# Kernel tuning notes

Measured on AMD Instinct MI355X. Metric: run time of the kernel, lower is better.

Reference implementation:

```python
import jax, jax.numpy as jnp
import numpy as np
import math

B, C, H, W = 8, 512, 32, 32
ENC = 1024
L2 = 64
NH = 8
GROUPS = 32
EPS = 1e-5

def group_norm(x, gamma, beta):
    # x: (B, C, L) GroupNorm with 32 groups (float32)
    b, c, l = x.shape
    xg = x.reshape(b, GROUPS, (c // GROUPS) * l)
    mean = xg.mean(-1, keepdims=True)
    var = xg.var(-1, keepdims=True)
    xn = ((xg - mean) * jax.lax.rsqrt(var + EPS)).reshape(b, c, l)
    return xn * gamma[None, :, None] + beta[None, :, None]

def conv1x1(w, bias, x):
    # conv_nd(1, in, out, 1): w (out, in), x (B, in, L) -> (B, out, L)
    return jnp.einsum('oc,bcl->bol', w, x) + bias[None, :, None]

def setup_inputs() -> dict:
    key = jax.random.key(0)
    ks = jax.random.split(key, 16)
    s = lambda fan_in: 1.0 / math.sqrt(fan_in)
    inp = {
        'x': jax.random.normal(ks[0], (B, C, H, W), jnp.float32),
        'xf_out': jax.random.normal(ks[1], (B, ENC, L2), jnp.float32),
        'obj_class_embedding': jax.random.normal(ks[2], (B, ENC, L2), jnp.float32),
        'obj_bbox_embedding': jax.random.normal(ks[3], (B, ENC, L2), jnp.float32),
        'image_patch_bbox_embedding': jax.random.normal(ks[4], (B, ENC, H * W), jnp.float32),
        'key_padding_mask': jax.random.bernoulli(ks[5], 0.3, (B, L2)),
        'qkv_w': jax.random.normal(ks[6], (3 * C, C), jnp.float32) * s(C),
        'qkv_b': jnp.zeros((3 * C,), jnp.float32),
        'g_qkv': jnp.ones((C,), jnp.float32),
        'b_qkv': jnp.zeros((C,), jnp.float32),
        'lc_w': jax.random.normal(ks[7], (2 * C, ENC), jnp.float32) * s(ENC),
        'lc_b': jnp.zeros((2 * C,), jnp.float32),
        'lp_w': jax.random.normal(ks[8], (C, ENC), jnp.float32) * s(ENC),
        'lp_b': jnp.zeros((C,), jnp.float32),
        'g_obj': jnp.ones((ENC,), jnp.float32),
        'b_obj': jnp.zeros((ENC,), jnp.float32),
        'g_lpos': jnp.ones((C,), jnp.float32),
        'b_lpos': jnp.zeros((C,), jnp.float32),
        'g_ipos': jnp.ones((C,), jnp.float32),
        'b_ipos': jnp.zeros((C,), jnp.float32),
        # proj_out is zero-initialized in the original (zero_module); use random
        # weights so the projection math is exercised non-trivially.
        'proj_w': jax.random.normal(ks[9], (C, C), jnp.float32) * s(C),
        'proj_b': jnp.zeros((C,), jnp.float32),
    }
    return inp

def reference(x, xf_out, obj_class_embedding, obj_bbox_embedding,
              image_patch_bbox_embedding, key_padding_mask,
              qkv_w, qkv_b, g_qkv, b_qkv, lc_w, lc_b, lp_w, lp_b,
              g_obj, b_obj, g_lpos, b_lpos, g_ipos, b_ipos, proj_w, proj_b):
    b, c, h, w = x.shape
    L1 = h * w
    d = C // NH
    xf = x.reshape(b, c, L1)

    qkv = conv1x1(qkv_w, qkv_b, group_norm(xf, g_qkv, b_qkv))  # (B, 3C, L1)
    q, k, v = jnp.split(qkv, 3, axis=1)
    q = q.reshape(b * NH, d, L1)
    k = k.reshape(b * NH, d, L1)
    v = v.reshape(b * NH, d, L1)

    ipp = group_norm(conv1x1(lp_w, lp_b, image_patch_bbox_embedding), g_ipos, b_ipos)
    ipp = ipp.reshape(b * NH, d, L1)

    q_img = jnp.concatenate([q, ipp], axis=1)  # (B*H, 2d, L1)
    k_img = jnp.concatenate([k, ipp], axis=1)

    lpe = group_norm(conv1x1(lp_w, lp_b, obj_bbox_embedding), g_lpos, b_lpos)
    lpe = lpe.reshape(b * NH, d, L2)

    lce = (xf_out + group_norm(obj_class_embedding, g_obj, b_obj)) / 2
    kl, vl = jnp.split(conv1x1(lc_w, lc_b, lce), 2, axis=1)
    kl = kl.reshape(b * NH, d, L2)
    vl = vl.reshape(b * NH, d, L2)
    k_layout = jnp.concatenate([kl, lpe], axis=1)  # (B*H, 2d, L2)

    k_mix = jnp.concatenate([k_img, k_layout], axis=2)  # (B*H, 2d, L1+L2)
    v_mix = jnp.concatenate([v, vl], axis=2)             # (B*H, d, L1+L2)

    mask = jnp.concatenate([jnp.zeros((b, L1), bool), key_padding_mask], axis=1)  # (B, L1+L2)

    scale = 1.0 / math.sqrt(math.sqrt(2 * C // NH))
    attn = jnp.einsum('bct,bcs->bts', q_img * scale, k_mix * scale)  # (B*H, L1, L1+L2)
    attn = attn.reshape(b, NH, L1, L1 + L2)
    attn = jnp.where(mask[:, None, None, :], -jnp.inf, attn)
    attn = jax.nn.softmax(attn.astype(jnp.float32), axis=-1).astype(attn.dtype)
    attn = attn.reshape(b * NH, L1, L1 + L2)

    out = jnp.einsum('bts,bcs->bct', attn, v_mix).reshape(b, C, L1)
    hproj = conv1x1(proj_w, proj_b, out)
    return (xf + hproj).reshape(b, c, h, w)
```

## Files before the change

### kernel.cpp

```cpp
#include <hip/hip_runtime.h>
#include <math.h>

#define NB 8
#define NC 512
#define NL1 1024
#define NL2 64
#define NLKV 1088
#define NENC 1024
#define EPSV 1e-5f
#define SCALE2 0.08838834764831845f
#define SCALE2Q 0.12752425f
#define DEFER_THR 11.5415603f

typedef _Float16 half8 __attribute__((ext_vector_type(8)));
typedef _Float16 half4 __attribute__((ext_vector_type(4)));
typedef __fp16 fp16x2 __attribute__((ext_vector_type(2)));
typedef float f32x4 __attribute__((ext_vector_type(4)));
typedef float f32x16 __attribute__((ext_vector_type(16)));

__device__ __forceinline__ void gload16(const _Float16* g, _Float16* l) {
  __builtin_amdgcn_global_load_lds(
      (const __attribute__((address_space(1))) void*)g,
      (__attribute__((address_space(3))) void*)l, 16, 0, 0);
}

__device__ __forceinline__ unsigned int pkrtz(float a, float b) {
  union { fp16x2 hh; unsigned int uu; } cv;
  cv.hh = __builtin_amdgcn_cvt_pkrtz(a, b);
  return cv.uu;
}

__device__ __forceinline__ float fast_exp2(float x) {
  return __builtin_amdgcn_exp2f(x);
}

__global__ __launch_bounds__(256) void k_init(
    const float* __restrict__ x, const float* __restrict__ obj,
    float* __restrict__ xm, float* __restrict__ xr,
    float* __restrict__ om, float* __restrict__ orr,
    const float* __restrict__ qkv_w, _Float16* __restrict__ w16qkv,
    const float* __restrict__ lp_w, _Float16* __restrict__ w16lp,
    const float* __restrict__ proj_w, _Float16* __restrict__ w16proj,
    const float* __restrict__ lc_w, _Float16* __restrict__ w16lc)
{
  int bid = blockIdx.x;
  if (bid < 512) {
    const float* p; float* meanp; float* rstdp; int n, bg;
    if (bid < 256) {
      bg = bid;
      int b = bg >> 5, g = bg & 31;
      p = x + ((size_t)b * 512 + (size_t)g * 16) * 1024;
      n = 16 * 1024; meanp = xm; rstdp = xr;
    } else {
      bg = bid - 256;
      int b = bg >> 5, g = bg & 31;
      p = obj + ((size_t)b * 1024 + (size_t)g * 32) * 64;
      n = 32 * 64; meanp = om; rstdp = orr;
    }
    float s = 0.f, s2 = 0.f;
    for (int i = threadIdx.x; i < n; i += 256) { float v = p[i]; s += v; s2 += v * v; }
    #pragma unroll
    for (int o = 32; o > 0; o >>= 1) { s += __shfl_down(s, o); s2 += __shfl_down(s2, o); }
    __shared__ float rs[4], rq[4];
    int lane = threadIdx.x & 63, w = threadIdx.x >> 6;
    if (lane == 0) { rs[w] = s; rq[w] = s2; }
    __syncthreads();
    if (threadIdx.x == 0) {
      float S = rs[0] + rs[1] + rs[2] + rs[3];
      float Q = rq[0] + rq[1] + rq[2] + rq[3];
      float m = S / n;
      float v = Q / n - m * m;
      if (v < 0.f) v = 0.f;
      meanp[bg] = m;
      rstdp[bg] = rsqrtf(v + EPSV);
    }
  } else {
    int cb = bid - 512;
    const float* s; _Float16* d; int i4;
    if (cb < 768)        { s = qkv_w;  d = w16qkv;  i4 = cb * 256 + threadIdx.x; }
    else if (cb < 1280)  { s = lp_w;   d = w16lp;   i4 = (cb - 768) * 256 + threadIdx.x; }
    else if (cb < 1536)  { s = proj_w; d = w16proj; i4 = (cb - 1280) * 256 + threadIdx.x; }
    else                 { s = lc_w;   d = w16lc;   i4 = (cb - 1536) * 256 + threadIdx.x; }
    float4 v = *(const float4*)&s[(size_t)i4 * 4];
    half4 o; o.x = (_Float16)v.x; o.y = (_Float16)v.y; o.z = (_Float16)v.z; o.w = (_Float16)v.w;
    *(half4*)&d[(size_t)i4 * 4] = o;
  }
}

__global__ __launch_bounds__(256) void k_prep(
    const float* __restrict__ x, const float* __restrict__ xm, const float* __restrict__ xr,
    const float* __restrict__ g_qkv, const float* __restrict__ b_qkv, _Float16* __restrict__ xT,
    const float* __restrict__ ipbe, _Float16* __restrict__ ipbeT,
    const float* __restrict__ xf_out, const float* __restrict__ obj_class,
    const float* __restrict__ obj_bbox,
    const float* __restrict__ om, const float* __restrict__ orr,
    const float* __restrict__ g_obj, const float* __restrict__ b_obj,
    _Float16* __restrict__ lceT, _Float16* __restrict__ objT)
{
  __shared__ _Float16 tile[64][72];
  const int bid = blockIdx.x;
  const int tl = threadIdx.x & 63;
  if (bid < 1024) {
    const int tt = bid & 15, ct = (bid >> 4) & 7, b = bid >> 7;
    const int c0 = ct * 64, t0 = tt * 64;
    const int cp = threadIdx.x >> 6;
    #pragma unroll
    for (int i = 0; i < 16; i++) {
      int c = c0 + i * 4 + cp;
      float v = x[((size_t)b * NC + c) * NL1 + t0 + tl];
      int g = c >> 4;
      float ga = g_qkv[c] * xr[b * 32 + g];
      float be = b_qkv[c] - xm[b * 32 + g] * ga;
      tile[tl][i * 4 + cp] = (_Float16)(v * ga + be);
    }
    __syncthreads();
    int tr = threadIdx.x >> 2, c16 = (threadIdx.x & 3) * 16;
    _Float16* dst = xT + ((size_t)b * 1024 + t0 + tr) * 512 + c0 + c16;
    *(half8*)dst = *(half8*)&tile[tr][c16];
    *(half8*)(dst + 8) = *(half8*)&tile[tr][c16 + 8];
  } else if (bid < 3072) {
    const int e2 = bid - 1024;
    const int tt = e2 & 15, et = (e2 >> 4) & 15, b = e2 >> 8;
    const int e0 = et * 64, t0 = tt * 64;
    const int ep = threadIdx.x >> 6;
    #pragma unroll
    for (int i = 0; i < 16; i++) {
      int e = e0 + i * 4 + ep;
      tile[tl][i * 4 + ep] = (_Float16)ipbe[((size_t)b * 1024 + e) * 1024 + t0 + tl];
    }
    __syncthreads();
    int tr = threadIdx.x >> 2, c16 = (threadIdx.x & 3) * 16;
    _Float16* d = ipbeT + ((size_t)b * 1024 + t0 + tr) * 1024 + e0 + c16;
    *(half8*)d = *(half8*)&tile[tr][c16];
    *(half8*)(d + 8) = *(half8*)&tile[tr][c16 + 8];
  } else {
    const int e2 = bid - 3072;
    const int et = e2 & 15, which = (e2 >> 4) & 1, b = e2 >> 5;
    const int e0 = et * 64;
    const int ep = threadIdx.x >> 6;
    if (which == 0) {
      #pragma unroll
      for (int i = 0; i < 16; i++) {
        int e = e0 + i * 4 + ep;
        size_t idx = ((size_t)b * 1024 + e) * 64 + tl;
        int g = e >> 5;
        float xn = (obj_class[idx] - om[b * 32 + g]) * orr[b * 32 + g] * g_obj[e] + b_obj[e];
        tile[tl][i * 4 + ep] = (_Float16)(0.5f * (xf_out[idx] + xn));
      }
    } else {
      #pragma unroll
      for (int i = 0; i < 16; i++) {
        int e = e0 + i * 4 + ep;
        tile[tl][i * 4 + ep] = (_Float16)obj_bbox[((size_t)b * 1024 + e) * 64 + tl];
      }
    }
    __syncthreads();
    int tr = threadIdx.x >> 2, c16 = (threadIdx.x & 3) * 16;
    _Float16* dst = (which == 0 ? lceT : objT) + ((size_t)b * 64 + tr) * 1024 + e0 + c16;
    *(half8*)dst = *(half8*)&tile[tr][c16];
    *(half8*)(dst + 8) = *(half8*)&tile[tr][c16 + 8];
  }
}

#define MFMA_CORE(KTOT)                                                                  \
  f32x4 acc[4][4];                                                                       \
  _Pragma("unroll") for (int i_ = 0; i_ < 4; i_++)                                       \
      _Pragma("unroll") for (int j_ = 0; j_ < 4; j_++) acc[i_][j_] = (f32x4)0.f;         \
  {                                                                                      \
    const int rsub = lane >> 3, csrc = (lane & 7) ^ rsub;                                \
    const int NT_ = (KTOT) / 64;                                                         \
    _Pragma("unroll") for (int i = 0; i < 4; i++) {                                      \
      int seg = w * 4 + i;                                                               \
      int row = seg * 8 + rsub;                                                          \
      gload16(Abase + (size_t)(m0 + row) * (KTOT) + csrc * 8, ldsA + seg * 512);         \
      gload16(Bbase + (size_t)(n0 + row) * (KTOT) + csrc * 8, ldsB + seg * 512);         \
    }                                                                                    \
    __syncthreads();                                                                     \
    int cur_ = 0;                                                                        \
    for (int t_ = 0; t_ < NT_; t_++) {                                                   \
      if (t_ + 1 < NT_) {                                                                \
        _Float16* da_ = ldsA + ((cur_ ^ 1) << 13);                                       \
        _Float16* db_ = ldsB + ((cur_ ^ 1) << 13);                                       \
        int kt = (t_ + 1) * 64;                                                          \
        _Pragma("unroll") for (int i = 0; i < 4; i++) {                                  \
          int seg = w * 4 + i;                                                           \
          int row = seg * 8 + rsub;                                                      \
          gload16(Abase + (size_t)(m0 + row) * (KTOT) + kt + csrc * 8, da_ + seg * 512); \
          gload16(Bbase + (size_t)(n0 + row) * (KTOT) + kt + csrc * 8, db_ + seg * 512); \
        }                                                                                \
      }                                                                                  \
      const char* ra_ = (const char*)(ldsA + (cur_ << 13));                              \
      const char* rb_ = (const char*)(ldsB + (cur_ << 13));                              \
      _Pragma("unroll") for (int kk = 0; kk < 2; kk++) {                                 \
        half8 af[4], bf[4];                                                              \
        _Pragma("unroll") for (int mb = 0; mb < 4; mb++) {                               \
          int row = wm + mb * 16 + l15;                                                  \
          af[mb] = *(const half8*)(ra_ + row * 128 +                                     \
                                   ((kk * 64 + lg * 16) ^ ((row & 7) << 4)));            \
        }                                                                                \
        _Pragma("unroll") for (int nb = 0; nb < 4; nb++) {                               \
          int row = wn + nb * 16 + l15;                                                  \
          bf[nb] = *(const half8*)(rb_ + row * 128 +                                     \
                                   ((kk * 64 + lg * 16) ^ ((row & 7) << 4)));            \
        }                                                                                \
        _Pragma("unroll") for (int mb = 0; mb < 4; mb++)                                 \
            _Pragma("unroll") for (int nb = 0; nb < 4; nb++)                             \
                acc[mb][nb] = __builtin_amdgcn_mfma_f32_16x16x32_f16(af[mb], bf[nb],     \
                                                                    acc[mb][nb], 0, 0, 0);\
      }                                                                                  \
      __syncthreads();                                                                   \
      cur_ ^= 1;                                                                         \
    }                                                                                    \
  }

#define MFMA_CORE_N64(KTOT)                                                              \
  f32x4 acc[4][2];                                                                       \
  _Pragma("unroll") for (int i_ = 0; i_ < 4; i_++)                                       \
      _Pragma("unroll") for (int j_ = 0; j_ < 2; j_++) acc[i_][j_] = (f32x4)0.f;         \
  {                                                                                      \
    const int rsub = lane >> 3, csrc = (lane & 7) ^ rsub;                                \
    const int NT_ = (KTOT) / 64;                                                         \
    _Pragma("unroll") for (int i = 0; i < 4; i++) {                                      \
      int seg = w * 4 + i;                                                               \
      int row = seg * 8 + rsub;                                                          \
      gload16(Abase + (size_t)(m0 + row) * (KTOT) + csrc * 8, ldsA + seg * 512);         \
    }                                                                                    \
    _Pragma("unroll") for (int i = 0; i < 2; i++) {                                      \
      int seg = w * 2 + i;                                                               \
      int row = seg * 8 + rsub;                                                          \
      gload16(Bbase + (size_t)row * (KTOT) + csrc * 8, ldsB + seg * 512);                \
    }                                                                                    \
    __syncthreads();                                                                     \
    int cur_ = 0;                                                                        \
    for (int t_ = 0; t_ < NT_; t_++) {                                                   \
      if (t_ + 1 < NT_) {                                                                \
        _Float16* da_ = ldsA + ((cur_ ^ 1) << 13);                                       \
        _Float16* db_ = ldsB + ((cur_ ^ 1) << 12);                                       \
        int kt = (t_ + 1) * 64;                                                          \
        _Pragma("unroll") for (int i = 0; i < 4; i++) {                                  \
          int seg = w * 4 + i;                                                           \
          int row = seg * 8 + rsub;                                                      \
          gload16(Abase + (size_t)(m0 + row) * (KTOT) + kt + csrc * 8, da_ + seg * 512); \
        }                                                                                \
        _Pragma("unroll") for (int i = 0; i < 2; i++) {                                  \
          int seg = w * 2 + i;                                                           \
          int row = seg * 8 + rsub;                                                      \
          gload16(Bbase + (size_t)row * (KTOT) + kt + csrc * 8, db_ + seg * 512);        \
        }                                                                                \
      }                                                                                  \
      const char* ra_ = (const char*)(ldsA + (cur_ << 13));                              \
      const char* rb_ = (const char*)(ldsB + (cur_ << 12));                              \
      _Pragma("unroll") for (int kk = 0; kk < 2; kk++) {                                 \
        half8 af[4], bf[2];                                                              \
        _Pragma("unroll") for (int mb = 0; mb < 4; mb++) {                               \
          int row = wm + mb * 16 + l15;                                                  \
          af[mb] = *(const half8*)(ra_ + row * 128 +                                     \
                                   ((kk * 64 + lg * 16) ^ ((row & 7) << 4)));            \
        }                                                                                \
        _Pragma("unroll") for (int nb = 0; nb < 2; nb++) {                               \
          int row = wn + nb * 16 + l15;                                                  \
          bf[nb] = *(const half8*)(rb_ + row * 128 +                                     \
                                   ((kk * 64 + lg * 16) ^ ((row & 7) << 4)));            \
        }                                                                                \
        _Pragma("unroll") for (int mb = 0; mb < 4; mb++)                                 \
            _Pragma("unroll") for (int nb = 0; nb < 2; nb++)                             \
                acc[mb][nb] = __builtin_amdgcn_mfma_f32_16x16x32_f16(af[mb], bf[nb],     \
                                                                    acc[mb][nb], 0, 0, 0);\
      }                                                                                  \
      __syncthreads();                                                                   \
      cur_ ^= 1;                                                                         \
    }                                                                                    \
  }

__global__ __launch_bounds__(256) void k_mfma_big(
    const _Float16* __restrict__ w16qkv, const float* __restrict__ qkv_b,
    const _Float16* __restrict__ xhatT,
    const _Float16* __restrict__ w16lp, const float* __restrict__ lp_b,
    const _Float16* __restrict__ ipbeT,
    const _Float16* __restrict__ w16lc, const float* __restrict__ lc_b,
    const _Float16* __restrict__ lceT, const _Float16* __restrict__ objT,
    const float* __restrict__ g_lpos, const float* __restrict__ b_lpos,
    _Float16* __restrict__ qT, _Float16* __restrict__ kT, _Float16* __restrict__ vT,
    _Float16* __restrict__ ipp16)
{
  __shared__ _Float16 smem[32768];
  const int bid0 = blockIdx.x;
  const int bid = (bid0 < 608) ? (bid0 + 768) : (bid0 - 608);
  const int tid = threadIdx.x, lane = tid & 63, w = tid >> 6;
  const int l15 = lane & 15, lg = lane >> 4;

  if (bid < 768) {
    const int nt = bid & 7, tt = bid >> 3;
    const int mt = tt % 12, b = tt / 12;
    const int m0 = mt * 128, n0 = nt * 128;
    _Float16* ldsA = smem;
    _Float16* ldsB = smem + 16384;
    const _Float16* Abase = w16qkv;
    const _Float16* Bbase = xhatT + (size_t)b * 1024 * 512;
    const int wm = (w >> 1) * 64, wn = (w & 1) * 64;
    MFMA_CORE(512)

    char* tb = (char*)smem;
    if (m0 < 1024) {
      const bool isq = (m0 < 512);
      const float qs = isq ? SCALE2Q : 1.f;
      #pragma unroll
      for (int mb = 0; mb < 4; mb++) {
        #pragma unroll
        for (int r = 0; r < 4; r++) {
          int mcol = wm + mb * 16 + lg * 4 + r;
          float bia = qkv_b[m0 + mcol];
          #pragma unroll
          for (int nb = 0; nb < 4; nb++) {
            int trow = wn + nb * 16 + l15;
            float val = (acc[mb][nb][r] + bia) * qs;
            *(_Float16*)(tb + ((trow * 256 + mcol * 2) ^ ((trow & 7) << 4))) = (_Float16)val;
          }
        }
      }
      __syncthreads();
      #pragma unroll
      for (int it = 0; it < 8; it++) {
        int e = it * 256 + tid;
        int trow = e >> 4, seg = e & 15;
        half8 v = *(const half8*)(tb + ((trow * 256 + seg * 16) ^ ((trow & 7) << 4)));
        if (isq) {
          int mq = m0 + seg * 8, hh = mq >> 6, dc = mq & 63;
          *(half8*)(qT + (((size_t)b * 8 + hh) * 1024 + n0 + trow) * 128 + dc) = v;
        } else {
          int mk = m0 - 512 + seg * 8, hh = mk >> 6, dc = mk & 63;
          *(half8*)(kT + (((size_t)b * 8 + hh) * 1088 + n0 + trow) * 128 + dc) = v;
        }
      }
    } else {
      #pragma unroll
      for (int mb = 0; mb < 4; mb++) {
        #pragma unroll
        for (int r = 0; r < 4; r++) {
          int mrow = wm + mb * 16 + lg * 4 + r;
          float bia = qkv_b[m0 + mrow];
          #pragma unroll
          for (int nb = 0; nb < 4; nb++) {
            int tcol = wn + nb * 16 + l15;
            *(_Float16*)(tb + ((mrow * 256 + tcol * 2) ^ ((mrow & 7) << 4))) =
                (_Float16)(acc[mb][nb][r] + bia);
          }
        }
      }
      __syncthreads();
      #pragma unroll
      for (int it = 0; it < 8; it++) {
        int e = it * 256 + tid;
        int mrow = e >> 4, seg = e & 15;
        half8 v = *(const half8*)(tb + ((mrow * 256 + seg * 16) ^ ((mrow & 7) << 4)));
        int mv = m0 - 1024 + mrow, hh = mv >> 6, dc = mv & 63;
        *(half8*)(vT + (((size_t)b * 8 + hh) * 64 + dc) * 1088 + n0 + seg * 8) = v;
      }
    }
  } else if (bid < 1280) {
    const int local = bid - 768;
    const int nt = local & 15, mt = (local >> 4) & 3, b = local >> 6;
    const int m0 = mt * 128, n0 = nt * 64;
    _Float16* ldsA = smem;
    _Float16* ldsB = smem + 16384;
    const _Float16* Abase = w16lp;
    const _Float16* Bbase = ipbeT + (size_t)b * 1024 * 1024 + (size_t)n0 * 1024;
    const int wm = (w >> 1) * 64, wn = (w & 1) * 32;
    MFMA_CORE_N64(1024)
    #pragma unroll
    for (int mb = 0; mb < 4; mb++) {
      #pragma unroll
      for (int r = 0; r < 4; r++) {
        int m = m0 + wm + mb * 16 + lg * 4 + r;
        float bia = lp_b[m];
        #pragma unroll
        for (int nb = 0; nb < 2; nb++) {
          int t = n0 + wn + nb * 16 + l15;
          ipp16[((size_t)b * NC + m) * NL1 + t] = (_Float16)(acc[mb][nb][r] + bia);
        }
      }
    }
  } else {
    const int local = bid - 1280;
    const int mt = local % 12, b = local / 12;
    const bool islc = (mt < 8);
    const int m0 = (islc ? mt : mt - 8) * 128;
    _Float16* ldsA = smem;
    _Float16* ldsB = smem + 16384;
    float (*red_s)[4] = (float(*)[4])(smem + 24576);
    float (*red_q)[4] = (float(*)[4])(smem + 24608);
    const _Float16* Abase = islc ? w16lc : w16lp;
    const float* bias = islc ? lc_b : lp_b;
    const _Float16* Bbase = (islc ? lceT : objT) + (size_t)b * 64 * 1024;
    const int wm = (w >> 1) * 64, wn = (w & 1) * 32;
    MFMA_CORE_N64(1024)

    if (islc) {
      #pragma unroll
      for (int mb = 0; mb < 4; mb++) {
        #pragma unroll
        for (int r = 0; r < 4; r++) {
          int m = m0 + wm + mb * 16 + lg * 4 + r;
          float bia = bias[m];
          #pragma unroll
          for (int nb = 0; nb < 2; nb++) {
            int l = wn + nb * 16 + l15;
            float val = acc[mb][nb][r] + bia;
            if (m < 512) {
              int h = m >> 6, dc = m & 63;
              kT[(((size_t)b * 8 + h) * 1088 + 1024 + l) * 128 + dc] = (_Float16)val;
            } else {
              int mv = m - 512, h = mv >> 6, dc = mv & 63;
              vT[(((size_t)b * 8 + h) * 64 + dc) * 1088 + 1024 + l] = (_Float16)val;
            }
          }
        }
      }
    } else {
      float vals[4][2][4];
      float ps[4], pq[4];
      #pragma unroll
      for (int mb = 0; mb < 4; mb++) {
        ps[mb] = 0.f; pq[mb] = 0.f;
        #pragma unroll
        for (int r = 0; r < 4; r++) {
          int m = m0 + wm + mb * 16 + lg * 4 + r;
          float bia = bias[m];
          #pragma unroll
          for (int nb = 0; nb < 2; nb++) {
            float val = acc[mb][nb][r] + bia;
            vals[mb][nb][r] = val;
            ps[mb] += val; pq[mb] += val * val;
          }
        }
      }
      #pragma unroll
      for (int mb = 0; mb < 4; mb++) {
        #pragma unroll
        for (int o = 32; o > 0; o >>= 1) {
          ps[mb] += __shfl_xor(ps[mb], o);
          pq[mb] += __shfl_xor(pq[mb], o);
        }
      }
      if (lane == 0) {
        #pragma unroll
        for (int mb = 0; mb < 4; mb++) { red_s[w][mb] = ps[mb]; red_q[w][mb] = pq[mb]; }
      }
      __syncthreads();
      const int wbase = (wm >> 6) * 2;
      #pragma unroll
      for (int mb = 0; mb < 4; mb++) {
        float S = red_s[wbase][mb] + red_s[wbase + 1][mb];
        float Q = red_q[wbase][mb] + red_q[wbase + 1][mb];
        float mean = S * (1.f / 1024.f);
        float var = Q * (1.f / 1024.f) - mean * mean;
        if (var < 0.f) var = 0.f;
        float rstd = rsqrtf(var + EPSV);
        #pragma unroll
        for (int r = 0; r < 4; r++) {
          int c = m0 + wm + mb * 16 + lg * 4 + r;
          float ga = g_lpos[c] * rstd;
          float be = b_lpos[c] - mean * ga;
          int hh = c >> 6, dc = c & 63;
          #pragma unroll
          for (int nb = 0; nb < 2; nb++) {
            int l = wn + nb * 16 + l15;
            float xn = vals[mb][nb][r] * ga + be;
            kT[(((size_t)b * 8 + hh) * 1088 + 1024 + l) * 128 + 64 + dc] = (_Float16)xn;
          }
        }
      }
    }
  }
}

__global__ __launch_bounds__(256) void k_mfma_proj(
    const _Float16* __restrict__ Abase, const float* __restrict__ bias,
    const _Float16* __restrict__ Ball, const float* __restrict__ xin,
    float* __restrict__ out)
{
  __shared__ _Float16 smem[24576];
  _Float16* ldsA = smem;
  _Float16* ldsB = smem + 16384;
  const int b = blockIdx.z, mt = blockIdx.y, nt = blockIdx.x;
  const int m0 = mt * 128, n0 = nt * 64;
  const _Float16* Bbase = Ball + (size_t)b * 1024 * 512 + (size_t)n0 * 512;
  const int tid = threadIdx.x, lane = tid & 63, w = tid >> 6;
  const int l15 = lane & 15, lg = lane >> 4;
  const int wm = (w >> 1) * 64, wn = (w & 1) * 32;
  MFMA_CORE_N64(512)
  #pragma unroll
  for (int mb = 0; mb < 4; mb++) {
    #pragma unroll
    for (int r = 0; r < 4; r++) {
      int m = m0 + wm + mb * 16 + lg * 4 + r;
      float bia = bias[m];
      #pragma unroll
      for (int nb = 0; nb < 2; nb++) {
        int t = n0 + wn + nb * 16 + l15;
        size_t idx = ((size_t)b * NC + m) * NL1 + t;
        out[idx] = xin[idx] + acc[mb][nb][r] + bia;
      }
    }
  }
}

__global__ __launch_bounds__(256) void k_ipp_fuse(
    const _Float16* __restrict__ raw,
    const float* __restrict__ gm, const float* __restrict__ gb,
    _Float16* __restrict__ qT, _Float16* __restrict__ kT)
{
  const int g = blockIdx.x, b = blockIdx.y;
  const int tid = threadIdx.x;
  const _Float16* p = raw + ((size_t)b * 512 + (size_t)g * 16) * 1024;
  const int t0 = tid * 4;

  float4 v[16];
  float s = 0.f, s2 = 0.f;
  #pragma unroll
  for (int c = 0; c < 16; c++) {
    half4 hv = *(const half4*)&p[(size_t)c * 1024 + t0];
    v[c].x = (float)hv.x; v[c].y = (float)hv.y; v[c].z = (float)hv.z; v[c].w = (float)hv.w;
    s += v[c].x + v[c].y + v[c].z + v[c].w;
    s2 += v[c].x * v[c].x + v[c].y * v[c].y + v[c].z * v[c].z + v[c].w * v[c].w;
  }
  #pragma unroll
  for (int o = 32; o > 0; o >>= 1) { s += __shfl_down(s, o); s2 += __shfl_down(s2, o); }
  __shared__ float rs[4], rq[4], stat[2];
  int lane = tid & 63, w = tid >> 6;
  if (lane == 0) { rs[w] = s; rq[w] = s2; }
  __syncthreads();
  if (tid == 0) {
    float S = rs[0] + rs[1] + rs[2] + rs[3];
    float Q = rq[0] + rq[1] + rq[2] + rq[3];
    float mn = S / 16384.f;
    float var = Q / 16384.f - mn * mn;
    if (var < 0.f) var = 0.f;
    stat[0] = mn; stat[1] = rsqrtf(var + EPSV);
  }
  __syncthreads();
  const float mn = stat[0], rstd = stat[1];

  float ga[16], be[16];
  #pragma unroll
  for (int c = 0; c < 16; c++) {
    ga[c] = gm[g * 16 + c] * rstd;
    be[c] = gb[g * 16 + c] - mn * ga[c];
  }

  const size_t bh = (size_t)b * 8 + (g >> 2);
  const int dcb = (g & 3) * 16;
  #pragma unroll
  for (int j = 0; j < 4; j++) {
    const int t = t0 + j;
    half8 k0, k1, q0, q1;
    #pragma unroll
    for (int c = 0; c < 8; c++) {
      float4 vc = v[c];
      float e = (j == 0) ? vc.x : (j == 1) ? vc.y : (j == 2) ? vc.z : vc.w;
      float xn = e * ga[c] + be[c];
      k0[c] = (_Float16)xn;
      q0[c] = (_Float16)(SCALE2Q * xn);
    }
    #pragma unroll
    for (int c = 8; c < 16; c++) {
      float4 vc = v[c];
      float e = (j == 0) ? vc.x : (j == 1) ? vc.y : (j == 2) ? vc.z : vc.w;
      float xn = e * ga[c] + be[c];
      k1[c - 8] = (_Float16)xn;
      q1[c - 8] = (_Float16)(SCALE2Q * xn);
    }
    _Float16* qd = qT + (bh * 1024 + t) * 128 + 64 + dcb;
    _Float16* kd = kT + (bh * 1088 + t) * 128 + 64 + dcb;
    *(half8*)qd = q0; *(half8*)(qd + 8) = q1;
    *(half8*)kd = k0; *(half8*)(kd + 8) = k1;
  }
}

__global__ __launch_bounds__(256) void k_attn_mfma(
    const _Float16* __restrict__ qT, const _Float16* __restrict__ kT,
    const _Float16* __restrict__ vT, const int* __restrict__ mask,
    _Float16* __restrict__ attnT)
{
  const int x = blockIdx.x & 7;
  const int k = blockIdx.x >> 3;
  const int bh = x + ((k >> 3) << 3);
  const int qt = k & 7;
  const int b = bh >> 3, h = bh & 7;
  const int tid = threadIdx.x;
  const int lane = tid & 63;
  const int w = tid >> 6;
  const int l31 = lane & 31;
  const int hi = lane >> 5;

  __shared__ _Float16 KsB[2 * 64 * 128];
  __shared__ _Float16 VtB[2 * 64 * 64];

  const int q = qt * 128 + w * 32 + l31;

  half8 aq[8];
  {
    const _Float16* qp = qT + ((size_t)bh * 1024 + q) * 128 + hi * 8;
    #pragma unroll
    for (int kst = 0; kst < 8; kst++) aq[kst] = *(const half8*)(qp + kst * 16);
  }

  unsigned int mbits = 0;
  {
    const int* mp = mask + b * 64;
    #pragma unroll
    for (int sb = 0; sb < 2; sb++) {
      #pragma unroll
      for (int reg = 0; reg < 16; reg++) {
        int s = sb * 32 + (reg & 3) + 8 * (reg >> 2) + 4 * hi;
        if (mp[s]) mbits |= 1u << (sb * 16 + reg);
      }
    }
  }

  f32x16 O0 = (f32x16)0.f, O1 = (f32x16)0.f;
  float m_run = -INFINITY, l_run = 0.f;

  const int kxor = (l31 & 7) << 4;
  const int ksrow_off = lane >> 4;
  const int kcsrc_base = lane & 15;
  const int vdc_off = lane >> 3;
  const int vcsrc_base = lane & 7;

#define STAGE_KV(T, KD, VD)                                                          \
  {                                                                                  \
    const int s0_ = (T) * 64;                                                        \
    _Pragma("unroll") for (int r = 0; r < 4; r++) {                                  \
      int seg = r * 4 + w;                                                           \
      int srow = seg * 4 + ksrow_off;                                                \
      int csrc = kcsrc_base ^ (srow & 7);                                            \
      gload16(kT + ((size_t)bh * 1088 + s0_ + srow) * 128 + csrc * 8, (KD) + seg * 512); \
    }                                                                                \
    _Pragma("unroll") for (int r = 0; r < 2; r++) {                                  \
      int seg = r * 4 + w;                                                           \
      int dc = seg * 8 + vdc_off;                                                    \
      int csrc = vcsrc_base ^ (dc & 7);                                              \
      gload16(vT + ((size_t)bh * 64 + dc) * 1088 + s0_ + csrc * 8, (VD) + seg * 512);  \
    }                                                                                \
  }

  STAGE_KV(0, KsB, VtB)
  asm volatile("s_waitcnt vmcnt(0)" ::: "memory");
  __builtin_amdgcn_s_barrier();

  int cur = 0;
  for (int t = 0; t < 17; t++) {
    if (t < 16) {
      _Float16* kd = KsB + ((cur ^ 1) << 13);
      _Float16* vd = VtB + ((cur ^ 1) << 12);
      STAGE_KV(t + 1, kd, vd)
    }
    const char* ksb = (const char*)(KsB + (cur << 13));
    const char* vtb = (const char*)(VtB + (cur << 12));

    f32x16 sc0 = (f32x16)0.f, sc1 = (f32x16)0.f;
    __builtin_amdgcn_s_setprio(1);
    #pragma unroll
    for (int kst = 0; kst < 8; kst++) {
      half8 kf0 = *(const half8*)(ksb + ((l31 * 256 + kst * 32 + hi * 16) ^ kxor));
      half8 kf1 = *(const half8*)(ksb + (((32 + l31) * 256 + kst * 32 + hi * 16) ^ kxor));
      sc0 = __builtin_amdgcn_mfma_f32_32x32x16_f16(kf0, aq[kst], sc0, 0, 0, 0);
      sc1 = __builtin_amdgcn_mfma_f32_32x32x16_f16(kf1, aq[kst], sc1, 0, 0, 0);
    }
    __builtin_amdgcn_s_setprio(0);

    if (t == 16) {
      #pragma unroll
      for (int i = 0; i < 16; i++) {
        if ((mbits >> i) & 1)        sc0[i] = -INFINITY;
        if ((mbits >> (16 + i)) & 1) sc1[i] = -INFINITY;
      }
    }

    float mx;
    {
      float a0 = fmaxf(fmaxf(sc0[0], sc0[1]), sc0[2]);
      float a1 = fmaxf(fmaxf(sc0[3], sc0[4]), sc0[5]);
      float a2 = fmaxf(fmaxf(sc0[6], sc0[7]), sc0[8]);
      float a3 = fmaxf(fmaxf(sc0[9], sc0[10]), sc0[11]);
      float a4 = fmaxf(fmaxf(sc0[12], sc0[13]), sc0[14]);
      float a5 = fmaxf(fmaxf(sc0[15], sc1[0]), sc1[1]);
      float a6 = fmaxf(fmaxf(sc1[2], sc1[3]), sc1[4]);
      float a7 = fmaxf(fmaxf(sc1[5], sc1[6]), sc1[7]);
      float a8 = fmaxf(fmaxf(sc1[8], sc1[9]), sc1[10]);
      float a9 = fmaxf(fmaxf(sc1[11], sc1[12]), sc1[13]);
      float aa = fmaxf(sc1[14], sc1[15]);
      float b0 = fmaxf(fmaxf(a0, a1), a2);
      float b1 = fmaxf(fmaxf(a3, a4), a5);
      float b2 = fmaxf(fmaxf(a6, a7), a8);
      float b3 = fmaxf(a9, aa);
      mx = fmaxf(fmaxf(b0, b1), fmaxf(b2, b3));
    }
    mx = fmaxf(mx, __shfl_xor(mx, 32));
    if (__all(mx <= m_run + DEFER_THR)) {
      float sum = 0.f;
      #pragma unroll
      for (int i = 0; i < 16; i++) { float p = fast_exp2(sc0[i] - m_run); sc0[i] = p; sum += p; }
      #pragma unroll
      for (int i = 0; i < 16; i++) { float p = fast_exp2(sc1[i] - m_run); sc1[i] = p; sum += p; }
      sum += __shfl_xor(sum, 32);
      l_run += sum;
    } else {
      float m_new = fmaxf(m_run, mx);
      float alpha = fast_exp2(m_run - m_new);
      float sum = 0.f;
      #pragma unroll
      for (int i = 0; i < 16; i++) { float p = fast_exp2(sc0[i] - m_new); sc0[i] = p; sum += p; }
      #pragma unroll
      for (int i = 0; i < 16; i++) { float p = fast_exp2(sc1[i] - m_new); sc1[i] = p; sum += p; }
      sum += __shfl_xor(sum, 32);
      l_run = l_run * alpha + sum;
      m_run = m_new;
      #pragma unroll
      for (int i = 0; i < 16; i++) { O0[i] *= alpha; O1[i] *= alpha; }
    }

    __builtin_amdgcn_s_setprio(1);
    #pragma unroll
    for (int sb = 0; sb < 2; sb++) {
      #pragma unroll
      for (int k2 = 0; k2 < 2; k2++) {
        const int kst = sb * 2 + k2;
        unsigned int pa0, pa1, pb0, pb1;
        if (sb == 0) {
          pa0 = pkrtz(sc0[8 * k2 + 0], sc0[8 * k2 + 1]);
          pa1 = pkrtz(sc0[8 * k2 + 2], sc0[8 * k2 + 3]);
          pb0 = pkrtz(sc0[8 * k2 + 4], sc0[8 * k2 + 5]);
          pb1 = pkrtz(sc0[8 * k2 + 6], sc0[8 * k2 + 7]);
        } else {
          pa0 = pkrtz(sc1[8 * k2 + 0], sc1[8 * k2 + 1]);
          pa1 = pkrtz(sc1[8 * k2 + 2], sc1[8 * k2 + 3]);
          pb0 = pkrtz(sc1[8 * k2 + 4], sc1[8 * k2 + 5]);
          pb1 = pkrtz(sc1[8 * k2 + 6], sc1[8 * k2 + 7]);
        }
        unsigned int keep0 = hi ? pb0 : pa0, keep1 = hi ? pb1 : pa1;
        unsigned int send0 = hi ? pa0 : pb0, send1 = hi ? pa1 : pb1;
        unsigned int recv0 = (unsigned int)__shfl_xor((int)send0, 32);
        unsigned int recv1 = (unsigned int)__shfl_xor((int)send1, 32);
        union { unsigned int u[4]; half8 hh; } pf;
        pf.u[0] = hi ? recv0 : keep0;
        pf.u[1] = hi ? recv1 : keep1;
        pf.u[2] = hi ? keep0 : recv0;
        pf.u[3] = hi ? keep1 : recv1;

        half8 vf0 = *(const half8*)(vtb + ((l31 * 128 + kst * 32 + hi * 16) ^ kxor));
        half8 vf1 = *(const half8*)(vtb + (((32 + l31) * 128 + kst * 32 + hi * 16) ^ kxor));
        O0 = __builtin_amdgcn_mfma_f32_32x32x16_f16(vf0, pf.hh, O0, 0, 0, 0);
        O1 = __builtin_amdgcn_mfma_f32_32x32x16_f16(vf1, pf.hh, O1, 0, 0, 0);
      }
    }
    __builtin_amdgcn_s_setprio(0);

    asm volatile("s_waitcnt vmcnt(0)" ::: "memory");
    __builtin_amdgcn_s_barrier();
    cur ^= 1;
  }

  float inv = 1.f / l_run;
  _Float16* op = attnT + ((size_t)b * 1024 + q) * 512 + h * 64;
  #pragma unroll
  for (int i = 0; i < 16; i += 2) {
    int dc = (i & 3) + 8 * (i >> 2) + 4 * hi;
    unsigned int c0 = pkrtz(O0[i] * inv, O0[i + 1] * inv);
    unsigned int c1 = pkrtz(O1[i] * inv, O1[i + 1] * inv);
    *(unsigned int*)(op + dc) = c0;
    *(unsigned int*)(op + 32 + dc) = c1;
  }
}

extern "C" void kernel_launch(void* const* d_in, const int* in_sizes, int n_in,
                              void* d_out, int out_size, void* d_ws, size_t ws_size,
                              hipStream_t stream) {
  const float* x         = (const float*)d_in[0];
  const float* xf_out    = (const float*)d_in[1];
  const float* obj_class = (const float*)d_in[2];
  const float* obj_bbox  = (const float*)d_in[3];
  const float* ipbe      = (const float*)d_in[4];
  const int*   mask      = (const int*)d_in[5];
  const float* qkv_w     = (const float*)d_in[6];
  const float* qkv_b     = (const float*)d_in[7];
  const float* g_qkv     = (const float*)d_in[8];
  const float* b_qkv     = (const float*)d_in[9];
  const float* lc_w      = (const float*)d_in[10];
  const float* lc_b      = (const float*)d_in[11];
  const float* lp_w      = (const float*)d_in[12];
  const float* lp_b      = (const float*)d_in[13];
  const float* g_obj     = (const float*)d_in[14];
  const float* b_obj     = (const float*)d_in[15];
  const float* g_lpos    = (const float*)d_in[16];
  const float* b_lpos    = (const float*)d_in[17];
  const float* g_ipos    = (const float*)d_in[18];
  const float* b_ipos    = (const float*)d_in[19];
  const float* proj_w    = (const float*)d_in[20];
  const float* proj_b    = (const float*)d_in[21];
  float* out = (float*)d_out;

  _Float16* f16b = (_Float16*)d_ws;
  _Float16* qT      = f16b;
  _Float16* kT      = qT + 8388608;
  _Float16* vT      = kT + 8912896;
  _Float16* xhatT   = vT + 4456448;
  _Float16* ipbeT   = xhatT + 4194304;
  _Float16* attnT   = ipbeT + 8388608;
  _Float16* w16qkv  = attnT + 4194304;
  _Float16* w16lp   = w16qkv + 786432;
  _Float16* w16proj = w16lp + 524288;
  _Float16* w16lc   = w16proj + 262144;
  _Float16* lceT    = w16lc + 1048576;
  _Float16* objT    = lceT + 524288;
  _Float16* ipp16   = objT + 524288;
  float* st = (float*)(ipp16 + 4194304);
  float* xm = st, * xr = st + 256, * om = st + 512, * orr = st + 768;

  dim3 blk(256);
  k_init<<<dim3(3072), blk, 0, stream>>>(x, obj_class, xm, xr, om, orr,
                                         qkv_w, w16qkv, lp_w, w16lp, proj_w, w16proj, lc_w, w16lc);
  k_prep<<<dim3(3328), blk, 0, stream>>>(x, xm, xr, g_qkv, b_qkv, xhatT,
                                         ipbe, ipbeT,
                                         xf_out, obj_class, obj_bbox, om, orr, g_obj, b_obj,
                                         lceT, objT);
  k_mfma_big<<<dim3(1376), blk, 0, stream>>>(w16qkv, qkv_b, xhatT,
                                             w16lp, lp_b, ipbeT,
                                             w16lc, lc_b, lceT, objT,
                                             g_lpos, b_lpos,
                                             qT, kT, vT, ipp16);
  k_ipp_fuse<<<dim3(32, 8), blk, 0, stream>>>(ipp16, g_ipos, b_ipos, qT, kT);
  k_attn_mfma<<<dim3(512), blk, 0, stream>>>(qT, kT, vT, mask, attnT);
  k_mfma_proj<<<dim3(16, 4, 8), blk, 0, stream>>>(w16proj, proj_b, attnT, x, out);
}
```

Before: 138.2 us.

## Software-pipeline attention QK and PV across tiles and retile the lp GEMM

The attention loop now computes the QK scores for tile t while running softmax and PV for tile t-1, using two alternating score register sets and a triple-buffered V tile in shared memory. The kernel also gets a launch bound of two blocks per CU. In k_mfma_big, the image-position GEMM moves from 128x64 tiles to 128x128 tiles, which cuts its block count from 512 to 256, and block ordering changes so the long lp-GEMM blocks are scheduled first. The aim is to overlap MFMA work with the exp and softmax math and to reduce per-block overhead, at the cost of extra registers and shared memory that could hurt occupancy or cause spills.

```diff
diff --git a/kernel.cpp b/kernel.cpp
--- a/kernel.cpp
+++ b/kernel.cpp
@@ -285,88 +285,18 @@
 {
   __shared__ _Float16 smem[32768];
   const int bid0 = blockIdx.x;
-  const int bid = (bid0 < 608) ? (bid0 + 768) : (bid0 - 608);
   const int tid = threadIdx.x, lane = tid & 63, w = tid >> 6;
   const int l15 = lane & 15, lg = lane >> 4;
 
-  if (bid < 768) {
-    const int nt = bid & 7, tt = bid >> 3;
-    const int mt = tt % 12, b = tt / 12;
+  if (bid0 < 256) {
+    const int nt = bid0 & 7, mt = (bid0 >> 3) & 3, b = bid0 >> 5;
     const int m0 = mt * 128, n0 = nt * 128;
     _Float16* ldsA = smem;
     _Float16* ldsB = smem + 16384;
-    const _Float16* Abase = w16qkv;
-    const _Float16* Bbase = xhatT + (size_t)b * 1024 * 512;
+    const _Float16* Abase = w16lp;
+    const _Float16* Bbase = ipbeT + (size_t)b * 1024 * 1024;
     const int wm = (w >> 1) * 64, wn = (w & 1) * 64;
-    MFMA_CORE(512)
-
-    char* tb = (char*)smem;
-    if (m0 < 1024) {
-      const bool isq = (m0 < 512);
-      const float qs = isq ? SCALE2Q : 1.f;
-      #pragma unroll
-      for (int mb = 0; mb < 4; mb++) {
-        #pragma unroll
-        for (int r = 0; r < 4; r++) {
-          int mcol = wm + mb * 16 + lg * 4 + r;
-          float bia = qkv_b[m0 + mcol];
-          #pragma unroll
-          for (int nb = 0; nb < 4; nb++) {
-            int trow = wn + nb * 16 + l15;
-            float val = (acc[mb][nb][r] + bia) * qs;
-            *(_Float16*)(tb + ((trow * 256 + mcol * 2) ^ ((trow & 7) << 4))) = (_Float16)val;
-          }
-        }
-      }
-      __syncthreads();
-      #pragma unroll
-      for (int it = 0; it < 8; it++) {
-        int e = it * 256 + tid;
-        int trow = e >> 4, seg = e & 15;
-        half8 v = *(const half8*)(tb + ((trow * 256 + seg * 16) ^ ((trow & 7) << 4)));
-        if (isq) {
-          int mq = m0 + seg * 8, hh = mq >> 6, dc = mq & 63;
-          *(half8*)(qT + (((size_t)b * 8 + hh) * 1024 + n0 + trow) * 128 + dc) = v;
-        } else {
-          int mk = m0 - 512 + seg * 8, hh = mk >> 6, dc = mk & 63;
-          *(half8*)(kT + (((size_t)b * 8 + hh) * 1088 + n0 + trow) * 128 + dc) = v;
-        }
-      }
-    } else {
-      #pragma unroll
-      for (int mb = 0; mb < 4; mb++) {
-        #pragma unroll
-        for (int r = 0; r < 4; r++) {
-          int mrow = wm + mb * 16 + lg * 4 + r;
-          float bia = qkv_b[m0 + mrow];
-          #pragma unroll
-          for (int nb = 0; nb < 4; nb++) {
-            int tcol = wn + nb * 16 + l15;
-            *(_Float16*)(tb + ((mrow * 256 + tcol * 2) ^ ((mrow & 7) << 4))) =
-                (_Float16)(acc[mb][nb][r] + bia);
-          }
-        }
-      }
-      __syncthreads();
-      #pragma unroll
-      for (int it = 0; it < 8; it++) {
-        int e = it * 256 + tid;
-        int mrow = e >> 4, seg = e & 15;
-        half8 v = *(const half8*)(tb + ((mrow * 256 + seg * 16) ^ ((mrow & 7) << 4)));
-        int mv = m0 - 1024 + mrow, hh = mv >> 6, dc = mv & 63;
-        *(half8*)(vT + (((size_t)b * 8 + hh) * 64 + dc) * 1088 + n0 + seg * 8) = v;
-      }
-    }
-  } else if (bid < 1280) {
-    const int local = bid - 768;
-    const int nt = local & 15, mt = (local >> 4) & 3, b = local >> 6;
-    const int m0 = mt * 128, n0 = nt * 64;
-    _Float16* ldsA = smem;
-    _Float16* ldsB = smem + 16384;
-    const _Float16* Abase = w16lp;
-    const _Float16* Bbase = ipbeT + (size_t)b * 1024 * 1024 + (size_t)n0 * 1024;
-    const int wm = (w >> 1) * 64, wn = (w & 1) * 32;
-    MFMA_CORE_N64(1024)
+    MFMA_CORE(1024)
     #pragma unroll
     for (int mb = 0; mb < 4; mb++) {
       #pragma unroll
@@ -374,14 +304,14 @@
         int m = m0 + wm + mb * 16 + lg * 4 + r;
         float bia = lp_b[m];
         #pragma unroll
-        for (int nb = 0; nb < 2; nb++) {
+        for (int nb = 0; nb < 4; nb++) {
           int t = n0 + wn + nb * 16 + l15;
           ipp16[((size_t)b * NC + m) * NL1 + t] = (_Float16)(acc[mb][nb][r] + bia);
         }
       }
     }
-  } else {
-    const int local = bid - 1280;
+  } else if (bid0 < 352) {
+    const int local = bid0 - 256;
     const int mt = local % 12, b = local / 12;
     const bool islc = (mt < 8);
     const int m0 = (islc ? mt : mt - 8) * 128;
@@ -469,6 +399,75 @@
             kT[(((size_t)b * 8 + hh) * 1088 + 1024 + l) * 128 + 64 + dc] = (_Float16)xn;
           }
         }
+      }
+    }
+  } else {
+    const int bid = bid0 - 352;
+    const int nt = bid & 7, tt = bid >> 3;
+    const int mt = tt % 12, b = tt / 12;
+    const int m0 = mt * 128, n0 = nt * 128;
+    _Float16* ldsA = smem;
+    _Float16* ldsB = smem + 16384;
+    const _Float16* Abase = w16qkv;
+    const _Float16* Bbase = xhatT + (size_t)b * 1024 * 512;
+    const int wm = (w >> 1) * 64, wn = (w & 1) * 64;
+    MFMA_CORE(512)
+
+    char* tb = (char*)smem;
+    if (m0 < 1024) {
+      const bool isq = (m0 < 512);
+      const float qs = isq ? SCALE2Q : 1.f;
+      #pragma unroll
+      for (int mb = 0; mb < 4; mb++) {
+        #pragma unroll
+        for (int r = 0; r < 4; r++) {
+          int mcol = wm + mb * 16 + lg * 4 + r;
+          float bia = qkv_b[m0 + mcol];
+          #pragma unroll
+          for (int nb = 0; nb < 4; nb++) {
+            int trow = wn + nb * 16 + l15;
+            float val = (acc[mb][nb][r] + bia) * qs;
+            *(_Float16*)(tb + ((trow * 256 + mcol * 2) ^ ((trow & 7) << 4))) = (_Float16)val;
+          }
+        }
+      }
+      __syncthreads();
+      #pragma unroll
+      for (int it = 0; it < 8; it++) {
+        int e = it * 256 + tid;
+        int trow = e >> 4, seg = e & 15;
+        half8 v = *(const half8*)(tb + ((trow * 256 + seg * 16) ^ ((trow & 7) << 4)));
+        if (isq) {
+          int mq = m0 + seg * 8, hh = mq >> 6, dc = mq & 63;
+          *(half8*)(qT + (((size_t)b * 8 + hh) * 1024 + n0 + trow) * 128 + dc) = v;
+        } else {
+          int mk = m0 - 512 + seg * 8, hh = mk >> 6, dc = mk & 63;
+          *(half8*)(kT + (((size_t)b * 8 + hh) * 1088 + n0 + trow) * 128 + dc) = v;
+        }
+      }
+    } else {
+      #pragma unroll
+      for (int mb = 0; mb < 4; mb++) {
+        #pragma unroll
+        for (int r = 0; r < 4; r++) {
+          int mrow = wm + mb * 16 + lg * 4 + r;
+          float bia = qkv_b[m0 + mrow];
+          #pragma unroll
+          for (int nb = 0; nb < 4; nb++) {
+            int tcol = wn + nb * 16 + l15;
+            *(_Float16*)(tb + ((mrow * 256 + tcol * 2) ^ ((mrow & 7) << 4))) =
+                (_Float16)(acc[mb][nb][r] + bia);
+          }
+        }
+      }
+      __syncthreads();
+      #pragma unroll
+      for (int it = 0; it < 8; it++) {
+        int e = it * 256 + tid;
+        int mrow = e >> 4, seg = e & 15;
+        half8 v = *(const half8*)(tb + ((mrow * 256 + seg * 16) ^ ((mrow & 7) << 4)));
+        int mv = m0 - 1024 + mrow, hh = mv >> 6, dc = mv & 63;
+        *(half8*)(vT + (((size_t)b * 8 + hh) * 64 + dc) * 1088 + n0 + seg * 8) = v;
       }
     }
   }
@@ -577,7 +576,7 @@
   }
 }
 
-__global__ __launch_bounds__(256) void k_attn_mfma(
+__global__ __launch_bounds__(256, 2) void k_attn_mfma(
     const _Float16* __restrict__ qT, const _Float16* __restrict__ kT,
     const _Float16* __restrict__ vT, const int* __restrict__ mask,
     _Float16* __restrict__ attnT)
@@ -594,7 +593,7 @@
   const int hi = lane >> 5;
 
   __shared__ _Float16 KsB[2 * 64 * 128];
-  __shared__ _Float16 VtB[2 * 64 * 64];
+  __shared__ _Float16 VtB[3 * 64 * 64];
 
   const int q = qt * 128 + w * 32 + l31;
 
@@ -619,6 +618,8 @@
   }
 
   f32x16 O0 = (f32x16)0.f, O1 = (f32x16)0.f;
+  f32x16 scA0 = (f32x16)0.f, scA1 = (f32x16)0.f;
+  f32x16 scB0 = (f32x16)0.f, scB1 = (f32x16)0.f;
   float m_run = -INFINITY, l_run = 0.f;
 
   const int kxor = (l31 & 7) << 4;
@@ -644,121 +645,121 @@
     }                                                                                \
   }
 
+#define ATTN_ITER(C0, C1, P0, P1, T)                                                 \
+  {                                                                                  \
+    const int T_ = (T);                                                              \
+    if (T_ <= 16) {                                                                  \
+      if (T_ <= 15) {                                                                \
+        _Float16* kd_ = KsB + (((T_ + 1) & 1) << 13);                                \
+        _Float16* vd_ = VtB + ((T_ + 1) % 3) * 4096;                                 \
+        STAGE_KV(T_ + 1, kd_, vd_)                                                   \
+      }                                                                              \
+      const char* ksb_ = (const char*)(KsB + ((T_ & 1) << 13));                      \
+      C0 = (f32x16)0.f; C1 = (f32x16)0.f;                                            \
+      __builtin_amdgcn_s_setprio(1);                                                 \
+      _Pragma("unroll") for (int kst = 0; kst < 8; kst++) {                          \
+        half8 kf0 = *(const half8*)(ksb_ + ((l31 * 256 + kst * 32 + hi * 16) ^ kxor)); \
+        half8 kf1 = *(const half8*)(ksb_ + (((32 + l31) * 256 + kst * 32 + hi * 16) ^ kxor)); \
+        C0 = __builtin_amdgcn_mfma_f32_32x32x16_f16(kf0, aq[kst], C0, 0, 0, 0);      \
+        C1 = __builtin_amdgcn_mfma_f32_32x32x16_f16(kf1, aq[kst], C1, 0, 0, 0);      \
+      }                                                                              \
+      __builtin_amdgcn_s_setprio(0);                                                 \
+    }                                                                                \
+    if (T_ >= 1) {                                                                   \
+      if (T_ == 17) {                                                                \
+        _Pragma("unroll") for (int i = 0; i < 16; i++) {                             \
+          if ((mbits >> i) & 1)        P0[i] = -INFINITY;                            \
+          if ((mbits >> (16 + i)) & 1) P1[i] = -INFINITY;                            \
+        }                                                                            \
+      }                                                                              \
+      float mx;                                                                      \
+      {                                                                              \
+        float a0 = fmaxf(fmaxf(P0[0], P0[1]), P0[2]);                                \
+        float a1 = fmaxf(fmaxf(P0[3], P0[4]), P0[5]);                                \
+        float a2 = fmaxf(fmaxf(P0[6], P0[7]), P0[8]);                                \
+        float a3 = fmaxf(fmaxf(P0[9], P0[10]), P0[11]);                              \
+        float a4 = fmaxf(fmaxf(P0[12], P0[13]), P0[14]);                             \
+        float a5 = fmaxf(fmaxf(P0[15], P1[0]), P1[1]);                               \
+        float a6 = fmaxf(fmaxf(P1[2], P1[3]), P1[4]);                                \
+        float a7 = fmaxf(fmaxf(P1[5], P1[6]), P1[7]);                                \
+        float a8 = fmaxf(fmaxf(P1[8], P1[9]), P1[10]);                               \
+        float a9 = fmaxf(fmaxf(P1[11], P1[12]), P1[13]);                             \
+        float aa = fmaxf(P1[14], P1[15]);                                            \
+        float b0 = fmaxf(fmaxf(a0, a1), a2);                                         \
+        float b1 = fmaxf(fmaxf(a3, a4), a5);                                         \
+        float b2 = fmaxf(fmaxf(a6, a7), a8);                                         \
+        float b3 = fmaxf(a9, aa);                                                    \
+        mx = fmaxf(fmaxf(b0, b1), fmaxf(b2, b3));                                    \
+      }                                                                              \
+      mx = fmaxf(mx, __shfl_xor(mx, 32));                                            \
+      if (__all(mx <= m_run + DEFER_THR)) {                                          \
+        float sum = 0.f;                                                             \
+        _Pragma("unroll") for (int i = 0; i < 16; i++) {                             \
+          float p = fast_exp2(P0[i] - m_run); P0[i] = p; sum += p; }                 \
+        _Pragma("unroll") for (int i = 0; i < 16; i++) {                             \
+          float p = fast_exp2(P1[i] - m_run); P1[i] = p; sum += p; }                 \
+        sum += __shfl_xor(sum, 32);                                                  \
+        l_run += sum;                                                                \
+      } else {                                                                       \
+        float m_new = fmaxf(m_run, mx);                                              \
+        float alpha = fast_exp2(m_run - m_new);                                      \
+        float sum = 0.f;                                                             \
+        _Pragma("unroll") for (int i = 0; i < 16; i++) {                             \
+          float p = fast_exp2(P0[i] - m_new); P0[i] = p; sum += p; }                 \
+        _Pragma("unroll") for (int i = 0; i < 16; i++) {                             \
+          float p = fast_exp2(P1[i] - m_new); P1[i] = p; sum += p; }                 \
+        sum += __shfl_xor(sum, 32);                                                  \
+        l_run = l_run * alpha + sum;                                                 \
+        m_run = m_new;                                                               \
+        _Pragma("unroll") for (int i = 0; i < 16; i++) { O0[i] *= alpha; O1[i] *= alpha; } \
+      }                                                                              \
+      const char* vtb_ = (const char*)(VtB + ((T_ - 1) % 3) * 4096);                 \
+      __builtin_amdgcn_s_setprio(1);                                                 \
+      _Pragma("unroll") for (int sb = 0; sb < 2; sb++) {                             \
+        _Pragma("unroll") for (int k2 = 0; k2 < 2; k2++) {                           \
+          const int kst = sb * 2 + k2;                                               \
+          unsigned int pa0, pa1, pb0, pb1;                                           \
+          if (sb == 0) {                                                             \
+            pa0 = pkrtz(P0[8 * k2 + 0], P0[8 * k2 + 1]);                             \
+            pa1 = pkrtz(P0[8 * k2 + 2], P0[8 * k2 + 3]);                             \
+            pb0 = pkrtz(P0[8 * k2 + 4], P0[8 * k2 + 5]);                             \
+            pb1 = pkrtz(P0[8 * k2 + 6], P0[8 * k2 + 7]);                             \
+          } else {                                                                   \
+            pa0 = pkrtz(P1[8 * k2 + 0], P1[8 * k2 + 1]);                             \
+            pa1 = pkrtz(P1[8 * k2 + 2], P1[8 * k2 + 3]);                             \
+            pb0 = pkrtz(P1[8 * k2 + 4], P1[8 * k2 + 5]);                             \
+            pb1 = pkrtz(P1[8 * k2 + 6], P1[8 * k2 + 7]);                             \
+          }                                                                          \
+          unsigned int keep0 = hi ? pb0 : pa0, keep1 = hi ? pb1 : pa1;               \
+          unsigned int send0 = hi ? pa0 : pb0, send1 = hi ? pa1 : pb1;               \
+          unsigned int recv0 = (unsigned int)__shfl_xor((int)send0, 32);             \
+          unsigned int recv1 = (unsigned int)__shfl_xor((int)send1, 32);             \
+          union { unsigned int u[4]; half8 hh; } pf;                                 \
+          pf.u[0] = hi ? recv0 : keep0;                                              \
+          pf.u[1] = hi ? recv1 : keep1;                                              \
+          pf.u[2] = hi ? keep0 : recv0;                                              \
+          pf.u[3] = hi ? keep1 : recv1;                                              \
+          half8 vf0 = *(const half8*)(vtb_ + ((l31 * 128 + kst * 32 + hi * 16) ^ kxor)); \
+          half8 vf1 = *(const half8*)(vtb_ + (((32 + l31) * 128 + kst * 32 + hi * 16) ^ kxor)); \
+          O0 = __builtin_amdgcn_mfma_f32_32x32x16_f16(vf0, pf.hh, O0, 0, 0, 0);      \
+          O1 = __builtin_amdgcn_mfma_f32_32x32x16_f16(vf1, pf.hh, O1, 0, 0, 0);      \
+        }                                                                            \
+      }                                                                              \
+      __builtin_amdgcn_s_setprio(0);                                                 \
+    }                                                                                \
+    if (T_ < 17) {                                                                   \
+      asm volatile("s_waitcnt vmcnt(0)" ::: "memory");                               \
+      __builtin_amdgcn_s_barrier();                                                  \
+    }                                                                                \
+  }
+
   STAGE_KV(0, KsB, VtB)
   asm volatile("s_waitcnt vmcnt(0)" ::: "memory");
   __builtin_amdgcn_s_barrier();
 
-  int cur = 0;
-  for (int t = 0; t < 17; t++) {
-    if (t < 16) {
-      _Float16* kd = KsB + ((cur ^ 1) << 13);
-      _Float16* vd = VtB + ((cur ^ 1) << 12);
-      STAGE_KV(t + 1, kd, vd)
-    }
-    const char* ksb = (const char*)(KsB + (cur << 13));
-    const char* vtb = (const char*)(VtB + (cur << 12));
-
-    f32x16 sc0 = (f32x16)0.f, sc1 = (f32x16)0.f;
-    __builtin_amdgcn_s_setprio(1);
-    #pragma unroll
-    for (int kst = 0; kst < 8; kst++) {
-      half8 kf0 = *(const half8*)(ksb + ((l31 * 256 + kst * 32 + hi * 16) ^ kxor));
-      half8 kf1 = *(const half8*)(ksb + (((32 + l31) * 256 + kst * 32 + hi * 16) ^ kxor));
-      sc0 = __builtin_amdgcn_mfma_f32_32x32x16_f16(kf0, aq[kst], sc0, 0, 0, 0);
-      sc1 = __builtin_amdgcn_mfma_f32_32x32x16_f16(kf1, aq[kst], sc1, 0, 0, 0);
-    }
-    __builtin_amdgcn_s_setprio(0);
-
-    if (t == 16) {
-      #pragma unroll
-      for (int i = 0; i < 16; i++) {
-        if ((mbits >> i) & 1)        sc0[i] = -INFINITY;
-        if ((mbits >> (16 + i)) & 1) sc1[i] = -INFINITY;
-      }
-    }
-
-    float mx;
-    {
-      float a0 = fmaxf(fmaxf(sc0[0], sc0[1]), sc0[2]);
-      float a1 = fmaxf(fmaxf(sc0[3], sc0[4]), sc0[5]);
-      float a2 = fmaxf(fmaxf(sc0[6], sc0[7]), sc0[8]);
-      float a3 = fmaxf(fmaxf(sc0[9], sc0[10]), sc0[11]);
-      float a4 = fmaxf(fmaxf(sc0[12], sc0[13]), sc0[14]);
-      float a5 = fmaxf(fmaxf(sc0[15], sc1[0]), sc1[1]);
-      float a6 = fmaxf(fmaxf(sc1[2], sc1[3]), sc1[4]);
-      float a7 = fmaxf(fmaxf(sc1[5], sc1[6]), sc1[7]);
-      float a8 = fmaxf(fmaxf(sc1[8], sc1[9]), sc1[10]);
-      float a9 = fmaxf(fmaxf(sc1[11], sc1[12]), sc1[13]);
-      float aa = fmaxf(sc1[14], sc1[15]);
-      float b0 = fmaxf(fmaxf(a0, a1), a2);
-      float b1 = fmaxf(fmaxf(a3, a4), a5);
-      float b2 = fmaxf(fmaxf(a6, a7), a8);
-      float b3 = fmaxf(a9, aa);
-      mx = fmaxf(fmaxf(b0, b1), fmaxf(b2, b3));
-    }
-    mx = fmaxf(mx, __shfl_xor(mx, 32));
-    if (__all(mx <= m_run + DEFER_THR)) {
-      float sum = 0.f;
-      #pragma unroll
-      for (int i = 0; i < 16; i++) { float p = fast_exp2(sc0[i] - m_run); sc0[i] = p; sum += p; }
-      #pragma unroll
-      for (int i = 0; i < 16; i++) { float p = fast_exp2(sc1[i] - m_run); sc1[i] = p; sum += p; }
-      sum += __shfl_xor(sum, 32);
-      l_run += sum;
-    } else {
-      float m_new = fmaxf(m_run, mx);
-      float alpha = fast_exp2(m_run - m_new);
-      float sum = 0.f;
-      #pragma unroll
-      for (int i = 0; i < 16; i++) { float p = fast_exp2(sc0[i] - m_new); sc0[i] = p; sum += p; }
-      #pragma unroll
-      for (int i = 0; i < 16; i++) { float p = fast_exp2(sc1[i] - m_new); sc1[i] = p; sum += p; }
-      sum += __shfl_xor(sum, 32);
-      l_run = l_run * alpha + sum;
-      m_run = m_new;
-      #pragma unroll
-      for (int i = 0; i < 16; i++) { O0[i] *= alpha; O1[i] *= alpha; }
-    }
-
-    __builtin_amdgcn_s_setprio(1);
-    #pragma unroll
-    for (int sb = 0; sb < 2; sb++) {
-      #pragma unroll
-      for (int k2 = 0; k2 < 2; k2++) {
-        const int kst = sb * 2 + k2;
-        unsigned int pa0, pa1, pb0, pb1;
-        if (sb == 0) {
-          pa0 = pkrtz(sc0[8 * k2 + 0], sc0[8 * k2 + 1]);
-          pa1 = pkrtz(sc0[8 * k2 + 2], sc0[8 * k2 + 3]);
-          pb0 = pkrtz(sc0[8 * k2 + 4], sc0[8 * k2 + 5]);
-          pb1 = pkrtz(sc0[8 * k2 + 6], sc0[8 * k2 + 7]);
-        } else {
-          pa0 = pkrtz(sc1[8 * k2 + 0], sc1[8 * k2 + 1]);
-          pa1 = pkrtz(sc1[8 * k2 + 2], sc1[8 * k2 + 3]);
-          pb0 = pkrtz(sc1[8 * k2 + 4], sc1[8 * k2 + 5]);
-          pb1 = pkrtz(sc1[8 * k2 + 6], sc1[8 * k2 + 7]);
-        }
-        unsigned int keep0 = hi ? pb0 : pa0, keep1 = hi ? pb1 : pa1;
-        unsigned int send0 = hi ? pa0 : pb0, send1 = hi ? pa1 : pb1;
-        unsigned int recv0 = (unsigned int)__shfl_xor((int)send0, 32);
-        unsigned int recv1 = (unsigned int)__shfl_xor((int)send1, 32);
-        union { unsigned int u[4]; half8 hh; } pf;
-        pf.u[0] = hi ? recv0 : keep0;
-        pf.u[1] = hi ? recv1 : keep1;
-        pf.u[2] = hi ? keep0 : recv0;
-        pf.u[3] = hi ? keep1 : recv1;
-
-        half8 vf0 = *(const half8*)(vtb + ((l31 * 128 + kst * 32 + hi * 16) ^ kxor));
-        half8 vf1 = *(const half8*)(vtb + (((32 + l31) * 128 + kst * 32 + hi * 16) ^ kxor));
-        O0 = __builtin_amdgcn_mfma_f32_32x32x16_f16(vf0, pf.hh, O0, 0, 0, 0);
-        O1 = __builtin_amdgcn_mfma_f32_32x32x16_f16(vf1, pf.hh, O1, 0, 0, 0);
-      }
-    }
-    __builtin_amdgcn_s_setprio(0);
-
-    asm volatile("s_waitcnt vmcnt(0)" ::: "memory");
-    __builtin_amdgcn_s_barrier();
-    cur ^= 1;
+  for (int t = 0; t < 18; t += 2) {
+    ATTN_ITER(scA0, scA1, scB0, scB1, t)
+    ATTN_ITER(scB0, scB1, scA0, scA1, t + 1)
   }
 
   float inv = 1.f / l_run;
@@ -824,7 +825,7 @@
                                          ipbe, ipbeT,
                                          xf_out, obj_class, obj_bbox, om, orr, g_obj, b_obj,
                                          lceT, objT);
-  k_mfma_big<<<dim3(1376), blk, 0, stream>>>(w16qkv, qkv_b, xhatT,
+  k_mfma_big<<<dim3(1120), blk, 0, stream>>>(w16qkv, qkv_b, xhatT,
                                              w16lp, lp_b, ipbeT,
                                              w16lc, lc_b, lceT, objT,
                                              g_lpos, b_lpos,
```

Measured after the change: 136.9 us. About the same (-1.0%).
